# Kernel optimization log

Measured on AMD Instinct MI355X. Metric: run time of the kernel, lower is better.

Reference implementation:

```python
import jax, jax.numpy as jnp
import numpy as np

N_TAXA = 32   # N taxa
K = 256       # particles
T = 16        # live subtrees at this step (t = N - r)
R = 16        # merges already done
S = 1024      # alignment sites
A = 4         # DNA alphabet
D = 64        # embedding dim
C = 16        # site-position feature dim
PRIOR_LEN = 0.1


def _expm4(M):
    """Matrix exponential of [..., A, A] via scaling-and-squaring + Taylor."""
    n_sq = 6
    Ms = M / (2.0 ** n_sq)
    I = jnp.eye(M.shape[-1], dtype=M.dtype)
    P = I + Ms
    Tm = Ms
    for i in range(2, 7):
        Tm = jnp.matmul(Tm, Ms) / i
        P = P + Tm
    for _ in range(n_sq):
        P = jnp.matmul(P, P)
    return P


def _stat_probs(emb_ExD, site_SxC, W_stat, W_site):
    # q_matrix_decoder.stat_probs_VxSxA: per-node, per-site stationary probs
    logits = emb_ExD @ W_stat                     # [E, A]
    logits = logits[:, None, :] + site_SxC @ W_site  # [E, S, A]
    return jax.nn.softmax(logits, axis=-1)


def setup_inputs() -> dict:
    key = jax.random.key(0)
    ks = jax.random.split(key, 10)
    ldf = np.zeros(2 * N_TAXA, np.float32)
    for n in range(2, 2 * N_TAXA):
        ldf[n] = ldf[n - 2] + np.log(n)
    return {
        "log_weight_K": jax.random.normal(ks[0], (K,), jnp.float32),
        "branch1_lengths_Kxr": jax.random.uniform(ks[1], (K, R), jnp.float32) * 0.2 + 1e-3,
        "branch2_lengths_Kxr": jax.random.uniform(ks[2], (K, R), jnp.float32) * 0.2 + 1e-3,
        "leaf_counts_Kxt": jnp.ones((K, T), jnp.int32),
        "embeddings_KxtxD": jax.random.normal(ks[3], (K, T, D), jnp.float32),
        "log_felsensteins_KxtxSxA": jax.nn.log_softmax(
            jax.random.normal(ks[4], (K, T, S, A), jnp.float32), axis=-1),
        "log_pi_K": jax.random.normal(ks[5], (K,), jnp.float32),
        "site_positions_SxC": jax.random.uniform(ks[6], (S, C), jnp.float32),
        "W_stat": jax.random.normal(ks[7], (D, A), jnp.float32) * 0.1,
        "W_site": jax.random.normal(ks[8], (C, A), jnp.float32) * 0.1,
        "log_double_factorials_2N": jnp.asarray(ldf),
    }


def reference(log_weight_K, branch1_lengths_Kxr, branch2_lengths_Kxr,
              leaf_counts_Kxt, embeddings_KxtxD, log_felsensteins_KxtxSxA,
              log_pi_K, site_positions_SxC, W_stat, W_site,
              log_double_factorials_2N):
    K_, T_, S_, A_ = log_felsensteins_KxtxSxA.shape
    key = jax.random.key(42)
    kres, ki, koff, ku1, ku2 = jax.random.split(key, 5)

    # ---- SMC categorical resampling over particles ----
    idxK = jax.random.categorical(kres, log_weight_K, shape=(K_,))
    b1r = branch1_lengths_Kxr[idxK]
    b2r = branch2_lengths_Kxr[idxK]
    lc = leaf_counts_Kxt[idxK]
    emb = embeddings_KxtxD[idxK]
    logf = log_felsensteins_KxtxSxA[idxK]
    prev_log_pi = log_pi_K[idxK]

    # ---- proposal (J=1): uniform pair + exponential branch lengths ----
    i = jax.random.randint(ki, (K_,), 0, T_)
    off = jax.random.randint(koff, (K_,), 1, T_)
    j = (i + off) % T_
    idx1 = jnp.minimum(i, j)
    idx2 = jnp.maximum(i, j)
    branch1 = -PRIOR_LEN * jnp.log(jax.random.uniform(ku1, (K_,), minval=1e-6, maxval=1.0))
    branch2 = -PRIOR_LEN * jnp.log(jax.random.uniform(ku2, (K_,), minval=1e-6, maxval=1.0))
    ar = jnp.arange(K_)
    new_emb = 0.5 * (emb[ar, idx1] + emb[ar, idx2])  # [K, D]
    log_v_plus = jnp.log(T_ * (T_ - 1) / 2.0)        # log #pairs

    # ---- merge: put merged value at idx1, move last slot into idx2, drop last ----
    def merge(arr, new_val):
        arr = arr.at[ar, idx1].set(new_val)
        arr = arr.at[ar, idx2].set(arr[ar, T_ - 1])
        return arr[:, :T_ - 1]

    lc_new = merge(lc, lc[ar, idx1] + lc[ar, idx2])   # [K, t-1]
    emb_new = merge(emb, new_emb)                     # [K, t-1, D]

    # ---- Felsenstein pruning step for the merged node ----
    stat = _stat_probs(new_emb, site_positions_SxC, W_stat, W_site)  # [K,S,A]
    Q = jnp.broadcast_to(stat[:, :, None, :], (K_, S_, A_, A_)) - jnp.eye(A_, dtype=stat.dtype)
    P1 = _expm4(Q * branch1[:, None, None, None])  # [K,S,A,A]
    P2 = _expm4(Q * branch2[:, None, None, None])
    f1 = jnp.exp(logf[ar, idx1])  # [K,S,A]
    f2 = jnp.exp(logf[ar, idx2])
    new_logf = (jnp.log(jnp.einsum('ksab,ksb->ksa', P1, f1) + 1e-30)
                + jnp.log(jnp.einsum('ksab,ksb->ksa', P2, f2) + 1e-30))
    logf_new = merge(logf, new_logf)  # [K, t-1, S, A]

    # ---- log pi over the forest: per-subtree likelihood + priors ----
    t_new = T_ - 1
    stat_all = _stat_probs(emb_new.reshape(K_ * t_new, -1), site_positions_SxC,
                           W_stat, W_site).reshape(K_, t_new, S_, A_)
    log_stat = jnp.log(stat_all)
    L = jnp.sum(jax.scipy.special.logsumexp(logf_new + log_stat, axis=-1), axis=-1)  # [K,t-1]
    topo_idx = jnp.clip(2 * lc_new - 3, 0, 2 * N_TAXA - 1)
    topo = -log_double_factorials_2N[topo_idx] * (lc_new >= 2).astype(L.dtype)
    b1_all = jnp.concatenate([b1r, branch1[:, None]], axis=1)  # [K, r+1]
    b2_all = jnp.concatenate([b2r, branch2[:, None]], axis=1)
    prior = (jnp.sum(-b1_all / PRIOR_LEN, axis=1) + jnp.sum(-b2_all / PRIOR_LEN, axis=1)
             - 2.0 * (b1_all.shape[1]) * jnp.log(jnp.asarray(PRIOR_LEN, L.dtype)))
    log_pi_new = jnp.sum(L + topo, axis=1) + prior

    # ---- importance weight ----
    log_v_minus = jnp.log(jnp.maximum(jnp.sum((lc_new > 1).astype(L.dtype), axis=1), 1.0))
    log_weight_new = log_pi_new - prev_log_pi + log_v_minus - log_v_plus
    return log_weight_new
```

## Files before the change

kernel.cpp:

```cpp
#include <hip/hip_runtime.h>
#include <stdint.h>


#define TF_ROT(x0,x1,r) { x0 += x1; x1 = ((x1<<(r))|(x1>>(32-(r)))); x1 ^= x0; }

__host__ __device__ inline void tf2x32(uint32_t k0, uint32_t k1,
                                       uint32_t x0, uint32_t x1,
                                       uint32_t& o0, uint32_t& o1) {
  uint32_t ks2 = k0 ^ k1 ^ 0x1BD11BDAu;
  x0 += k0; x1 += k1;
  TF_ROT(x0,x1,13) TF_ROT(x0,x1,15) TF_ROT(x0,x1,26) TF_ROT(x0,x1,6)
  x0 += k1; x1 += ks2 + 1u;
  TF_ROT(x0,x1,17) TF_ROT(x0,x1,29) TF_ROT(x0,x1,16) TF_ROT(x0,x1,24)
  x0 += ks2; x1 += k0 + 2u;
  TF_ROT(x0,x1,13) TF_ROT(x0,x1,15) TF_ROT(x0,x1,26) TF_ROT(x0,x1,6)
  x0 += k0; x1 += k1 + 3u;
  TF_ROT(x0,x1,17) TF_ROT(x0,x1,29) TF_ROT(x0,x1,16) TF_ROT(x0,x1,24)
  x0 += k1; x1 += ks2 + 4u;
  TF_ROT(x0,x1,13) TF_ROT(x0,x1,15) TF_ROT(x0,x1,26) TF_ROT(x0,x1,6)
  x0 += ks2; x1 += k0 + 5u;
  o0 = x0; o1 = x1;
}

struct Keys {
  uint32_t kres0, kres1;
  uint32_t k2i0, k2i1;
  uint32_t k1o0, k1o1;
  uint32_t k2o0, k2o1;
  uint32_t ku10, ku11;
  uint32_t ku20, ku21;
};

__device__ inline uint32_t rb_fold(uint32_t k0, uint32_t k1, uint32_t i) {
  uint32_t o0, o1;
  tf2x32(k0, k1, 0u, i, o0, o1);
  return o0 ^ o1;
}

__device__ inline float u01f(uint32_t b) {
  return __uint_as_float((b >> 9) | 0x3F800000u) - 1.0f;
}

#define TINYF 1.17549435e-38f

__global__ __launch_bounds__(256) void k_site(const float* __restrict__ site,
                                              const float* __restrict__ Wsite,
                                              float* __restrict__ slw) {
  int s = blockIdx.x * 256 + threadIdx.x;
  float a0 = 0.f, a1 = 0.f, a2 = 0.f, a3 = 0.f;
#pragma unroll
  for (int c = 0; c < 16; c++) {
    float sc = site[s * 16 + c];
    a0 += sc * Wsite[c * 4 + 0];
    a1 += sc * Wsite[c * 4 + 1];
    a2 += sc * Wsite[c * 4 + 2];
    a3 += sc * Wsite[c * 4 + 3];
  }
  float4 v; v.x = a0; v.y = a1; v.z = a2; v.w = a3;
  ((float4*)slw)[s] = v;
}

__global__ __launch_bounds__(256) void k_setup(
    const float* __restrict__ logw, const float* __restrict__ b1r,
    const float* __restrict__ b2r, const int* __restrict__ lc,
    const float* __restrict__ emb, const float* __restrict__ logpi,
    const float* __restrict__ Wstat, const float* __restrict__ ldf,
    float* __restrict__ nlw, float* __restrict__ w1w, float* __restrict__ w2w,
    float* __restrict__ cw, int* __restrict__ pw, int* __restrict__ i1w,
    int* __restrict__ i2w, Keys kk) {
  int k = blockIdx.x, tid = threadIdx.x;
  __shared__ float sval[256];
  __shared__ int   sidx[256];
  __shared__ int   sh_i1, sh_i2;

  {
    uint32_t idx = (uint32_t)(k * 256 + tid);
    uint32_t b = rb_fold(kk.kres0, kk.kres1, idx);
    float u = fmaxf(TINYF, u01f(b) + TINYF);
    float g = -logf(-logf(u));
    sval[tid] = g + logw[tid];
    sidx[tid] = tid;
  }
  __syncthreads();
  for (int st = 128; st > 0; st >>= 1) {
    if (tid < st) {
      float va = sval[tid], vb = sval[tid + st];
      int ia = sidx[tid], ib = sidx[tid + st];
      if (vb > va || (vb == va && ib < ia)) { sval[tid] = vb; sidx[tid] = ib; }
    }
    __syncthreads();
  }
  int p = sidx[0];

  if (tid == 0) {
    uint32_t i = rb_fold(kk.k2i0, kk.k2i1, (uint32_t)k) & 15u;
    uint32_t h = rb_fold(kk.k1o0, kk.k1o1, (uint32_t)k) % 15u;
    uint32_t l = rb_fold(kk.k2o0, kk.k2o1, (uint32_t)k) % 15u;
    uint32_t off = 1u + (h + l) % 15u;
    uint32_t j = (i + off) & 15u;
    int i1 = (int)(i < j ? i : j);
    int i2 = (int)(i < j ? j : i);
    sh_i1 = i1; sh_i2 = i2;

    const float SUBR = 1.0f - 1e-6f;
    float u1 = fmaxf(1e-6f, u01f(rb_fold(kk.ku10, kk.ku11, (uint32_t)k)) * SUBR + 1e-6f);
    float u2 = fmaxf(1e-6f, u01f(rb_fold(kk.ku20, kk.ku21, (uint32_t)k)) * SUBR + 1e-6f);
    float b1 = -0.1f * logf(u1);
    float b2 = -0.1f * logf(u2);
    w1w[k] = 1.0f - expf(-b1);
    w2w[k] = 1.0f - expf(-b2);
    i1w[k] = i1; i2w[k] = i2; pw[k] = p;

    float sb = b1 + b2;
    for (int r = 0; r < 16; r++) sb += b1r[p * 16 + r] + b2r[p * 16 + r];
    float prior = -sb / 0.1f - 34.0f * logf(0.1f);

    float topo_sum = 0.0f; int cnt = 0;
    for (int t = 0; t < 15; t++) {
      int lct;
      if (t == i1)      lct = lc[p * 16 + i1] + lc[p * 16 + i2];
      else if (t == i2) lct = lc[p * 16 + 15];
      else              lct = lc[p * 16 + t];
      int ti = 2 * lct - 3; ti = ti < 0 ? 0 : (ti > 63 ? 63 : ti);
      if (lct >= 2) topo_sum -= ldf[ti];
      if (lct > 1) cnt++;
    }
    float log_v_minus = logf(fmaxf((float)cnt, 1.0f));
    float log_v_plus = logf(120.0f);
    cw[k] = prior + topo_sum - logpi[p] + log_v_minus - log_v_plus;
  }
  __syncthreads();

  if (tid < 60) {
    int t = tid >> 2, a = tid & 3;
    int i1 = sh_i1, i2 = sh_i2;
    int p2 = sidx[0];
    float acc = 0.0f;
    if (t == i1) {
      const float* e1 = emb + ((size_t)p2 * 16 + i1) * 64;
      const float* e2 = emb + ((size_t)p2 * 16 + i2) * 64;
      for (int d = 0; d < 64; d++) acc += 0.5f * (e1[d] + e2[d]) * Wstat[d * 4 + a];
    } else {
      int src = (t == i2) ? 15 : t;
      const float* e = emb + ((size_t)p2 * 16 + src) * 64;
      for (int d = 0; d < 64; d++) acc += e[d] * Wstat[d * 4 + a];
    }
    nlw[k * 60 + t * 4 + a] = acc;
  }
}

__global__ __launch_bounds__(256) void k_main(
    const float* __restrict__ lfg, const float* __restrict__ slw,
    const float* __restrict__ nlw, const float* __restrict__ w1w,
    const float* __restrict__ w2w, const int* __restrict__ pw,
    const int* __restrict__ i1w, const int* __restrict__ i2w,
    float* __restrict__ Lpart) {
  int k = blockIdx.y, bx = blockIdx.x, tid = threadIdx.x;
  int s = bx * 256 + tid;
  __shared__ float snl[60];
  __shared__ float sred[15 * 4];
  if (tid < 60) snl[tid] = nlw[k * 60 + tid];
  __syncthreads();
  int p = pw[k], i1 = i1w[k], i2 = i2w[k];
  float w1 = w1w[k], w2 = w2w[k];
  const float4 sl = ((const float4*)slw)[s];
  const float* base = lfg + (size_t)p * 16 * 1024 * 4;

  float q0 = snl[i1 * 4 + 0] + sl.x, q1 = snl[i1 * 4 + 1] + sl.y;
  float q2 = snl[i1 * 4 + 2] + sl.z, q3 = snl[i1 * 4 + 3] + sl.w;
  float qm = fmaxf(fmaxf(q0, q1), fmaxf(q2, q3));
  float e0 = expf(q0 - qm), e1 = expf(q1 - qm), e2 = expf(q2 - qm), e3 = expf(q3 - qm);
  float inv = 1.0f / (e0 + e1 + e2 + e3);
  float st0 = e0 * inv, st1 = e1 * inv, st2 = e2 * inv, st3 = e3 * inv;

  float4 lf1 = *(const float4*)(base + ((size_t)i1 * 1024 + s) * 4);
  float4 lf2 = *(const float4*)(base + ((size_t)i2 * 1024 + s) * 4);
  float f10 = expf(lf1.x), f11 = expf(lf1.y), f12 = expf(lf1.z), f13 = expf(lf1.w);
  float f20 = expf(lf2.x), f21 = expf(lf2.y), f22 = expf(lf2.z), f23 = expf(lf2.w);
  float dot1 = st0 * f10 + st1 * f11 + st2 * f12 + st3 * f13;
  float dot2 = st0 * f20 + st1 * f21 + st2 * f22 + st3 * f23;
  float om1 = 1.0f - w1, om2 = 1.0f - w2;
  float n0 = logf(om1 * f10 + w1 * dot1 + 1e-30f) + logf(om2 * f20 + w2 * dot2 + 1e-30f);
  float n1 = logf(om1 * f11 + w1 * dot1 + 1e-30f) + logf(om2 * f21 + w2 * dot2 + 1e-30f);
  float n2 = logf(om1 * f12 + w1 * dot1 + 1e-30f) + logf(om2 * f22 + w2 * dot2 + 1e-30f);
  float n3 = logf(om1 * f13 + w1 * dot1 + 1e-30f) + logf(om2 * f23 + w2 * dot2 + 1e-30f);

#pragma unroll
  for (int t = 0; t < 15; t++) {
    float l0 = snl[t * 4 + 0] + sl.x, l1 = snl[t * 4 + 1] + sl.y;
    float l2 = snl[t * 4 + 2] + sl.z, l3 = snl[t * 4 + 3] + sl.w;
    float lm = fmaxf(fmaxf(l0, l1), fmaxf(l2, l3));
    float lse_l = lm + logf(expf(l0 - lm) + expf(l1 - lm) + expf(l2 - lm) + expf(l3 - lm));
    float x0, x1, x2, x3;
    if (t == i1) { x0 = n0; x1 = n1; x2 = n2; x3 = n3; }
    else {
      int srct = (t == i2) ? 15 : t;
      float4 lf = *(const float4*)(base + ((size_t)srct * 1024 + s) * 4);
      x0 = lf.x; x1 = lf.y; x2 = lf.z; x3 = lf.w;
    }
    x0 += l0; x1 += l1; x2 += l2; x3 += l3;
    float xm = fmaxf(fmaxf(x0, x1), fmaxf(x2, x3));
    float contr = xm + logf(expf(x0 - xm) + expf(x1 - xm) + expf(x2 - xm) + expf(x3 - xm)) - lse_l;
    float v = contr;
    for (int o = 32; o > 0; o >>= 1) v += __shfl_down(v, o, 64);
    if ((tid & 63) == 0) sred[t * 4 + (tid >> 6)] = v;
  }
  __syncthreads();
  if (tid < 15) {
    float sum = sred[tid * 4 + 0] + sred[tid * 4 + 1] + sred[tid * 4 + 2] + sred[tid * 4 + 3];
    Lpart[(size_t)k * 60 + bx * 15 + tid] = sum;
  }
}

__global__ __launch_bounds__(256) void k_final(const float* __restrict__ cw,
                                               const float* __restrict__ Lpart,
                                               float* __restrict__ out) {
  int k = threadIdx.x;
  float sum = cw[k];
  for (int q = 0; q < 60; q++) sum += Lpart[k * 60 + q];
  out[k] = sum;
}

extern "C" void kernel_launch(void* const* d_in, const int* in_sizes, int n_in,
                              void* d_out, int out_size, void* d_ws, size_t ws_size,
                              hipStream_t stream) {
  const float* logw  = (const float*)d_in[0];
  const float* b1r   = (const float*)d_in[1];
  const float* b2r   = (const float*)d_in[2];
  const int*   lc    = (const int*)d_in[3];
  const float* emb   = (const float*)d_in[4];
  const float* lfg   = (const float*)d_in[5];
  const float* logpi = (const float*)d_in[6];
  const float* site  = (const float*)d_in[7];
  const float* Wstat = (const float*)d_in[8];
  const float* Wsite = (const float*)d_in[9];
  const float* ldf   = (const float*)d_in[10];

  char* w = (char*)d_ws;
  float* slw   = (float*)w; w += 1024 * 4 * 4;
  float* nlw   = (float*)w; w += 256 * 60 * 4;
  float* w1w   = (float*)w; w += 256 * 4;
  float* w2w   = (float*)w; w += 256 * 4;
  float* cw    = (float*)w; w += 256 * 4;
  int*   pw    = (int*)w;   w += 256 * 4;
  int*   i1w   = (int*)w;   w += 256 * 4;
  int*   i2w   = (int*)w;   w += 256 * 4;
  float* Lpart = (float*)w; w += 256 * 60 * 4;

  uint32_t S0[5], S1[5];
  for (uint32_t i = 0; i < 5; i++) tf2x32(0u, 42u, 0u, i, S0[i], S1[i]);
  Keys kk;
  kk.kres0 = S0[0]; kk.kres1 = S1[0];
  kk.ku10  = S0[3]; kk.ku11  = S1[3];
  kk.ku20  = S0[4]; kk.ku21  = S1[4];
  {
    uint32_t a0, a1, b0, b1;
    tf2x32(S0[1], S1[1], 0u, 0u, a0, a1);
    tf2x32(S0[1], S1[1], 0u, 1u, b0, b1);
    (void)a0; (void)a1;
    kk.k2i0 = b0; kk.k2i1 = b1;
  }
  {
    uint32_t a0, a1, b0, b1;
    tf2x32(S0[2], S1[2], 0u, 0u, a0, a1);
    tf2x32(S0[2], S1[2], 0u, 1u, b0, b1);
    kk.k1o0 = a0; kk.k1o1 = a1;
    kk.k2o0 = b0; kk.k2o1 = b1;
  }

  k_site<<<4, 256, 0, stream>>>(site, Wsite, slw);
  k_setup<<<256, 256, 0, stream>>>(logw, b1r, b2r, lc, emb, logpi, Wstat, ldf,
                                   nlw, w1w, w2w, cw, pw, i1w, i2w, kk);
  dim3 g(4, 256);
  k_main<<<g, 256, 0, stream>>>(lfg, slw, nlw, w1w, w2w, pw, i1w, i2w, Lpart);
  k_final<<<1, 256, 0, stream>>>(cw, Lpart, (float*)d_out);
}
```

Before: 143.3 us.

## Precompute per-parent subtree likelihoods and reuse across particles, factor softmax exps

Adds a kernel that computes the per-site log-likelihood contribution for all 16 subtrees of every source particle p, independent of the resampled particle index. A final per-particle kernel then only evaluates the merged subtree, subtracts the two consumed subtrees' contributions, and adds the precomputed sum. Softmax and log-sum-exp are rewritten as products of exponentials (exp of site logits times exp of node logits), with fast __expf/__logf intrinsics. This removes most per-particle transcendental work, at the cost of possible overflow/precision issues from dropping max-subtraction and from the intrinsics.

```diff
diff --git a/kernel.cpp b/kernel.cpp
--- a/kernel.cpp
+++ b/kernel.cpp
@@ -43,9 +43,9 @@
 
 #define TINYF 1.17549435e-38f
 
-__global__ __launch_bounds__(256) void k_site(const float* __restrict__ site,
-                                              const float* __restrict__ Wsite,
-                                              float* __restrict__ slw) {
+__global__ __launch_bounds__(256) void k_esl(const float* __restrict__ site,
+                                             const float* __restrict__ Wsite,
+                                             float* __restrict__ eslw) {
   int s = blockIdx.x * 256 + threadIdx.x;
   float a0 = 0.f, a1 = 0.f, a2 = 0.f, a3 = 0.f;
 #pragma unroll
@@ -56,8 +56,8 @@
     a2 += sc * Wsite[c * 4 + 2];
     a3 += sc * Wsite[c * 4 + 3];
   }
-  float4 v; v.x = a0; v.y = a1; v.z = a2; v.w = a3;
-  ((float4*)slw)[s] = v;
+  float4 v; v.x = __expf(a0); v.y = __expf(a1); v.z = __expf(a2); v.w = __expf(a3);
+  ((float4*)eslw)[s] = v;
 }
 
 __global__ __launch_bounds__(256) void k_setup(
@@ -65,7 +65,7 @@
     const float* __restrict__ b2r, const int* __restrict__ lc,
     const float* __restrict__ emb, const float* __restrict__ logpi,
     const float* __restrict__ Wstat, const float* __restrict__ ldf,
-    float* __restrict__ nlw, float* __restrict__ w1w, float* __restrict__ w2w,
+    float* __restrict__ enlm, float* __restrict__ w1w, float* __restrict__ w2w,
     float* __restrict__ cw, int* __restrict__ pw, int* __restrict__ i1w,
     int* __restrict__ i2w, Keys kk) {
   int k = blockIdx.x, tid = threadIdx.x;
@@ -74,8 +74,7 @@
   __shared__ int   sh_i1, sh_i2;
 
   {
-    uint32_t idx = (uint32_t)(k * 256 + tid);
-    uint32_t b = rb_fold(kk.kres0, kk.kres1, idx);
+    uint32_t b = rb_fold(kk.kres0, kk.kres1, (uint32_t)(k * 256 + tid));
     float u = fmaxf(TINYF, u01f(b) + TINYF);
     float g = -logf(-logf(u));
     sval[tid] = g + logw[tid];
@@ -131,94 +130,105 @@
   }
   __syncthreads();
 
-  if (tid < 60) {
+  if (tid < 4) {
+    int a = tid, i1 = sh_i1, i2 = sh_i2, p2 = sidx[0];
+    const float* e1 = emb + ((size_t)p2 * 16 + i1) * 64;
+    const float* e2 = emb + ((size_t)p2 * 16 + i2) * 64;
+    float acc = 0.0f;
+    for (int d = 0; d < 64; d++) acc += 0.5f * (e1[d] + e2[d]) * Wstat[d * 4 + a];
+    enlm[k * 4 + a] = __expf(acc);
+  }
+}
+
+__global__ __launch_bounds__(256) void k_lorig(
+    const float* __restrict__ lfg, const float* __restrict__ eslw,
+    const float* __restrict__ emb, const float* __restrict__ Wstat,
+    float* __restrict__ Lpart) {
+  int p = blockIdx.y, sblk = blockIdx.x, tid = threadIdx.x;
+  __shared__ float enl[64];
+  __shared__ float sred[16 * 4];
+  if (tid < 64) {
     int t = tid >> 2, a = tid & 3;
-    int i1 = sh_i1, i2 = sh_i2;
-    int p2 = sidx[0];
+    const float* e = emb + ((size_t)p * 16 + t) * 64;
     float acc = 0.0f;
-    if (t == i1) {
-      const float* e1 = emb + ((size_t)p2 * 16 + i1) * 64;
-      const float* e2 = emb + ((size_t)p2 * 16 + i2) * 64;
-      for (int d = 0; d < 64; d++) acc += 0.5f * (e1[d] + e2[d]) * Wstat[d * 4 + a];
-    } else {
-      int src = (t == i2) ? 15 : t;
-      const float* e = emb + ((size_t)p2 * 16 + src) * 64;
-      for (int d = 0; d < 64; d++) acc += e[d] * Wstat[d * 4 + a];
-    }
-    nlw[k * 60 + t * 4 + a] = acc;
-  }
-}
-
-__global__ __launch_bounds__(256) void k_main(
-    const float* __restrict__ lfg, const float* __restrict__ slw,
-    const float* __restrict__ nlw, const float* __restrict__ w1w,
+    for (int d = 0; d < 64; d++) acc += e[d] * Wstat[d * 4 + a];
+    enl[tid] = __expf(acc);
+  }
+  __syncthreads();
+  int s = sblk * 256 + tid;
+  const float4 esl = ((const float4*)eslw)[s];
+  const float* base = lfg + (size_t)p * 65536;
+
+  float acc[16];
+#pragma unroll
+  for (int t = 0; t < 16; t++) {
+    float4 lf = *(const float4*)(base + t * 4096 + s * 4);
+    float w0 = enl[t * 4 + 0] * esl.x, w1 = enl[t * 4 + 1] * esl.y;
+    float w2 = enl[t * 4 + 2] * esl.z, w3 = enl[t * 4 + 3] * esl.w;
+    float S1 = w0 + w1 + w2 + w3;
+    float S2 = __expf(lf.x) * w0 + __expf(lf.y) * w1 +
+               __expf(lf.z) * w2 + __expf(lf.w) * w3;
+    acc[t] = __logf(S2) - __logf(S1);
+  }
+#pragma unroll
+  for (int t = 0; t < 16; t++) {
+    float v = acc[t];
+    for (int o = 32; o > 0; o >>= 1) v += __shfl_down(v, o, 64);
+    if ((tid & 63) == 0) sred[t * 4 + (tid >> 6)] = v;
+  }
+  __syncthreads();
+  if (tid < 16) {
+    float s4 = sred[tid * 4 + 0] + sred[tid * 4 + 1] + sred[tid * 4 + 2] + sred[tid * 4 + 3];
+    Lpart[((size_t)p * 4 + sblk) * 16 + tid] = s4;
+  }
+}
+
+__global__ __launch_bounds__(1024) void k_fin(
+    const float* __restrict__ lfg, const float* __restrict__ eslw,
+    const float* __restrict__ enlm, const float* __restrict__ w1w,
     const float* __restrict__ w2w, const int* __restrict__ pw,
     const int* __restrict__ i1w, const int* __restrict__ i2w,
-    float* __restrict__ Lpart) {
-  int k = blockIdx.y, bx = blockIdx.x, tid = threadIdx.x;
-  int s = bx * 256 + tid;
-  __shared__ float snl[60];
-  __shared__ float sred[15 * 4];
-  if (tid < 60) snl[tid] = nlw[k * 60 + tid];
-  __syncthreads();
+    const float* __restrict__ cw, const float* __restrict__ Lpart,
+    float* __restrict__ out) {
+  int k = blockIdx.x, tid = threadIdx.x;
+  __shared__ float sred[16];
   int p = pw[k], i1 = i1w[k], i2 = i2w[k];
   float w1 = w1w[k], w2 = w2w[k];
-  const float4 sl = ((const float4*)slw)[s];
-  const float* base = lfg + (size_t)p * 16 * 1024 * 4;
-
-  float q0 = snl[i1 * 4 + 0] + sl.x, q1 = snl[i1 * 4 + 1] + sl.y;
-  float q2 = snl[i1 * 4 + 2] + sl.z, q3 = snl[i1 * 4 + 3] + sl.w;
-  float qm = fmaxf(fmaxf(q0, q1), fmaxf(q2, q3));
-  float e0 = expf(q0 - qm), e1 = expf(q1 - qm), e2 = expf(q2 - qm), e3 = expf(q3 - qm);
-  float inv = 1.0f / (e0 + e1 + e2 + e3);
-  float st0 = e0 * inv, st1 = e1 * inv, st2 = e2 * inv, st3 = e3 * inv;
-
-  float4 lf1 = *(const float4*)(base + ((size_t)i1 * 1024 + s) * 4);
-  float4 lf2 = *(const float4*)(base + ((size_t)i2 * 1024 + s) * 4);
-  float f10 = expf(lf1.x), f11 = expf(lf1.y), f12 = expf(lf1.z), f13 = expf(lf1.w);
-  float f20 = expf(lf2.x), f21 = expf(lf2.y), f22 = expf(lf2.z), f23 = expf(lf2.w);
-  float dot1 = st0 * f10 + st1 * f11 + st2 * f12 + st3 * f13;
-  float dot2 = st0 * f20 + st1 * f21 + st2 * f22 + st3 * f23;
   float om1 = 1.0f - w1, om2 = 1.0f - w2;
-  float n0 = logf(om1 * f10 + w1 * dot1 + 1e-30f) + logf(om2 * f20 + w2 * dot2 + 1e-30f);
-  float n1 = logf(om1 * f11 + w1 * dot1 + 1e-30f) + logf(om2 * f21 + w2 * dot2 + 1e-30f);
-  float n2 = logf(om1 * f12 + w1 * dot1 + 1e-30f) + logf(om2 * f22 + w2 * dot2 + 1e-30f);
-  float n3 = logf(om1 * f13 + w1 * dot1 + 1e-30f) + logf(om2 * f23 + w2 * dot2 + 1e-30f);
-
-#pragma unroll
-  for (int t = 0; t < 15; t++) {
-    float l0 = snl[t * 4 + 0] + sl.x, l1 = snl[t * 4 + 1] + sl.y;
-    float l2 = snl[t * 4 + 2] + sl.z, l3 = snl[t * 4 + 3] + sl.w;
-    float lm = fmaxf(fmaxf(l0, l1), fmaxf(l2, l3));
-    float lse_l = lm + logf(expf(l0 - lm) + expf(l1 - lm) + expf(l2 - lm) + expf(l3 - lm));
-    float x0, x1, x2, x3;
-    if (t == i1) { x0 = n0; x1 = n1; x2 = n2; x3 = n3; }
-    else {
-      int srct = (t == i2) ? 15 : t;
-      float4 lf = *(const float4*)(base + ((size_t)srct * 1024 + s) * 4);
-      x0 = lf.x; x1 = lf.y; x2 = lf.z; x3 = lf.w;
-    }
-    x0 += l0; x1 += l1; x2 += l2; x3 += l3;
-    float xm = fmaxf(fmaxf(x0, x1), fmaxf(x2, x3));
-    float contr = xm + logf(expf(x0 - xm) + expf(x1 - xm) + expf(x2 - xm) + expf(x3 - xm)) - lse_l;
-    float v = contr;
-    for (int o = 32; o > 0; o >>= 1) v += __shfl_down(v, o, 64);
-    if ((tid & 63) == 0) sred[t * 4 + (tid >> 6)] = v;
-  }
-  __syncthreads();
-  if (tid < 15) {
-    float sum = sred[tid * 4 + 0] + sred[tid * 4 + 1] + sred[tid * 4 + 2] + sred[tid * 4 + 3];
-    Lpart[(size_t)k * 60 + bx * 15 + tid] = sum;
-  }
-}
-
-__global__ __launch_bounds__(256) void k_final(const float* __restrict__ cw,
-                                               const float* __restrict__ Lpart,
-                                               float* __restrict__ out) {
-  int k = threadIdx.x;
-  float sum = cw[k];
-  for (int q = 0; q < 60; q++) sum += Lpart[k * 60 + q];
-  out[k] = sum;
+  float m0 = enlm[k * 4 + 0], m1 = enlm[k * 4 + 1];
+  float m2 = enlm[k * 4 + 2], m3 = enlm[k * 4 + 3];
+  const float* base = lfg + (size_t)p * 65536;
+
+  int s = tid;
+  const float4 esl = ((const float4*)eslw)[s];
+  float t0 = m0 * esl.x, t1 = m1 * esl.y, t2 = m2 * esl.z, t3 = m3 * esl.w;
+  float T = t0 + t1 + t2 + t3;
+  float invT = 1.0f / T;
+  float4 lf1 = *(const float4*)(base + i1 * 4096 + s * 4);
+  float4 lf2 = *(const float4*)(base + i2 * 4096 + s * 4);
+  float f10 = __expf(lf1.x), f11 = __expf(lf1.y), f12 = __expf(lf1.z), f13 = __expf(lf1.w);
+  float f20 = __expf(lf2.x), f21 = __expf(lf2.y), f22 = __expf(lf2.z), f23 = __expf(lf2.w);
+  float dot1 = (t0 * f10 + t1 * f11 + t2 * f12 + t3 * f13) * invT;
+  float dot2 = (t0 * f20 + t1 * f21 + t2 * f22 + t3 * f23) * invT;
+  float n0 = __logf(om1 * f10 + w1 * dot1 + 1e-30f) + __logf(om2 * f20 + w2 * dot2 + 1e-30f);
+  float n1 = __logf(om1 * f11 + w1 * dot1 + 1e-30f) + __logf(om2 * f21 + w2 * dot2 + 1e-30f);
+  float n2 = __logf(om1 * f12 + w1 * dot1 + 1e-30f) + __logf(om2 * f22 + w2 * dot2 + 1e-30f);
+  float n3 = __logf(om1 * f13 + w1 * dot1 + 1e-30f) + __logf(om2 * f23 + w2 * dot2 + 1e-30f);
+  float S2 = __expf(n0) * t0 + __expf(n1) * t1 + __expf(n2) * t2 + __expf(n3) * t3;
+  float tot = __logf(S2) - __logf(T);
+
+  for (int o = 32; o > 0; o >>= 1) tot += __shfl_down(tot, o, 64);
+  if ((tid & 63) == 0) sred[tid >> 6] = tot;
+  __syncthreads();
+  if (tid == 0) {
+    float site_sum = 0.0f;
+    for (int q = 0; q < 16; q++) site_sum += sred[q];
+    const float* Lp = Lpart + (size_t)p * 64;
+    float Ls = 0.0f;
+    for (int q = 0; q < 64; q++) Ls += Lp[q];
+    for (int sb = 0; sb < 4; sb++) Ls -= Lp[sb * 16 + i1] + Lp[sb * 16 + i2];
+    out[k] = cw[k] + Ls + site_sum;
+  }
 }
 
 extern "C" void kernel_launch(void* const* d_in, const int* in_sizes, int n_in,
@@ -237,15 +247,15 @@
   const float* ldf   = (const float*)d_in[10];
 
   char* w = (char*)d_ws;
-  float* slw   = (float*)w; w += 1024 * 4 * 4;
-  float* nlw   = (float*)w; w += 256 * 60 * 4;
+  float* eslw  = (float*)w; w += 1024 * 4 * 4;
+  float* enlm  = (float*)w; w += 256 * 4 * 4;
   float* w1w   = (float*)w; w += 256 * 4;
   float* w2w   = (float*)w; w += 256 * 4;
   float* cw    = (float*)w; w += 256 * 4;
   int*   pw    = (int*)w;   w += 256 * 4;
   int*   i1w   = (int*)w;   w += 256 * 4;
   int*   i2w   = (int*)w;   w += 256 * 4;
-  float* Lpart = (float*)w; w += 256 * 60 * 4;
+  float* Lpart = (float*)w; w += 256 * 64 * 4;
 
   uint32_t S0[5], S1[5];
   for (uint32_t i = 0; i < 5; i++) tf2x32(0u, 42u, 0u, i, S0[i], S1[i]);
@@ -268,10 +278,11 @@
     kk.k2o0 = b0; kk.k2o1 = b1;
   }
 
-  k_site<<<4, 256, 0, stream>>>(site, Wsite, slw);
+  k_esl<<<4, 256, 0, stream>>>(site, Wsite, eslw);
   k_setup<<<256, 256, 0, stream>>>(logw, b1r, b2r, lc, emb, logpi, Wstat, ldf,
-                                   nlw, w1w, w2w, cw, pw, i1w, i2w, kk);
-  dim3 g(4, 256);
-  k_main<<<g, 256, 0, stream>>>(lfg, slw, nlw, w1w, w2w, pw, i1w, i2w, Lpart);
-  k_final<<<1, 256, 0, stream>>>(cw, Lpart, (float*)d_out);
-}
+                                   enlm, w1w, w2w, cw, pw, i1w, i2w, kk);
+  dim3 gC(4, 256);
+  k_lorig<<<gC, 256, 0, stream>>>(lfg, eslw, emb, Wstat, Lpart);
+  k_fin<<<256, 1024, 0, stream>>>(lfg, eslw, enlm, w1w, w2w, pw, i1w, i2w,
+                                  cw, Lpart, (float*)d_out);
+}
```

Measured after the change: 134.1 us. 6.4% less time.
